# Performance work log

Measured on AMD Instinct MI355X. Metric: run time of the kernel, lower is better.

The kernel has to match this reference:

```python
import jax, jax.numpy as jnp
import numpy as np
import math

B, S, HID = 2, 2048, 2048
H, KVH, D = 16, 4, 128
EPS = 1e-6
THETA = 10000.0


def _rope_tables(key):
    inv_freq = 1.0 / (THETA ** (jnp.arange(0, D, 2, dtype=jnp.float32) / D))  # [D/2]
    pos = jnp.arange(S, dtype=jnp.float32)
    freqs = pos[:, None] * inv_freq[None, :]            # [S, D/2]
    emb = jnp.concatenate([freqs, freqs], axis=-1)      # [S, D]
    cos = jnp.broadcast_to(jnp.cos(emb)[None], (B, S, D))
    sin = jnp.broadcast_to(jnp.sin(emb)[None], (B, S, D))
    return cos, sin


def setup_inputs() -> dict:
    key = jax.random.key(0)
    ks = jax.random.split(key, 6)
    hidden_states = jax.random.normal(ks[0], (B, S, HID), dtype=jnp.float32)
    # causal additive mask, broadcastable to [B, H, S, S]
    causal = jnp.tril(jnp.ones((S, S), dtype=jnp.bool_))
    attention_mask = jnp.where(causal, 0.0, jnp.finfo(jnp.float32).min)[None, None]
    cos, sin = _rope_tables(key)
    sc = 0.02
    Wq = jax.random.normal(ks[1], (HID, H * D), dtype=jnp.float32) * sc
    Wk = jax.random.normal(ks[2], (HID, KVH * D), dtype=jnp.float32) * sc
    Wv = jax.random.normal(ks[3], (HID, KVH * D), dtype=jnp.float32) * sc
    Wo = jax.random.normal(ks[4], (H * D, HID), dtype=jnp.float32) * sc
    q_norm_w = jnp.ones((D,), dtype=jnp.float32)
    k_norm_w = jnp.ones((D,), dtype=jnp.float32)
    return dict(hidden_states=hidden_states, attention_mask=attention_mask,
                cos=cos, sin=sin, Wq=Wq, Wk=Wk, Wv=Wv, Wo=Wo,
                q_norm_w=q_norm_w, k_norm_w=k_norm_w)


def _rms_norm(x, w, eps=EPS):
    dt = x.dtype
    xf = x.astype(jnp.float32)
    var = jnp.mean(xf * xf, axis=-1, keepdims=True)
    return (w * (xf * jax.lax.rsqrt(var + eps)).astype(dt)).astype(dt)


def _rotate_half(x):
    x1, x2 = jnp.split(x, 2, axis=-1)
    return jnp.concatenate([-x2, x1], axis=-1)


def reference(hidden_states, attention_mask, cos, sin, Wq, Wk, Wv, Wo, q_norm_w, k_norm_w):
    b, s, _ = hidden_states.shape
    q = (hidden_states @ Wq).reshape(b, s, H, D)
    k = (hidden_states @ Wk).reshape(b, s, KVH, D)
    v = (hidden_states @ Wv).reshape(b, s, KVH, D)
    q = _rms_norm(q, q_norm_w).transpose(0, 2, 1, 3)   # [B,H,S,D]
    k = _rms_norm(k, k_norm_w).transpose(0, 2, 1, 3)   # [B,KVH,S,D]
    v = v.transpose(0, 2, 1, 3)
    # RoPE: cos/sin [B,S,D] -> unsqueeze head dim
    c = cos[:, None]
    sn = sin[:, None]
    q = q * c + _rotate_half(q) * sn
    k = k * c + _rotate_half(k) * sn
    # repeat_kv for GQA
    n_rep = H // KVH
    k = jnp.repeat(k, n_rep, axis=1)
    v = jnp.repeat(v, n_rep, axis=1)
    scores = jnp.einsum('bhqd,bhkd->bhqk', q, k) / math.sqrt(D)
    scores = scores + attention_mask
    attn = jax.nn.softmax(scores.astype(jnp.float32), axis=-1).astype(q.dtype)
    out = jnp.einsum('bhqk,bhkd->bhqd', attn, v)
    out = out.transpose(0, 2, 1, 3).reshape(b, s, H * D)
    return out @ Wo
```

## Files before the change

### kernel.cpp

```cpp
#include <hip/hip_runtime.h>
#include <math.h>

#define B_ 2
#define S_ 2048
#define HID_ 2048
#define H_ 16
#define KVH_ 4
#define D_ 128

typedef __bf16 bf16x8 __attribute__((ext_vector_type(8)));
typedef float f32x4 __attribute__((ext_vector_type(4)));

__device__ __forceinline__ unsigned short f2bf(float x) {
  union { float f; unsigned u; } cv;
  cv.f = x;
  unsigned u = cv.u;
  u += 0x7FFFu + ((u >> 16) & 1u);
  return (unsigned short)(u >> 16);
}

__global__ __launch_bounds__(256) void convert_bf16_kernel(
    const float* __restrict__ in, unsigned short* __restrict__ out) {
  const size_t i = ((size_t)blockIdx.x * 256 + threadIdx.x) * 8;
  const float4 v0 = *reinterpret_cast<const float4*>(&in[i]);
  const float4 v1 = *reinterpret_cast<const float4*>(&in[i + 4]);
  ushort4 o0, o1;
  o0.x = f2bf(v0.x); o0.y = f2bf(v0.y); o0.z = f2bf(v0.z); o0.w = f2bf(v0.w);
  o1.x = f2bf(v1.x); o1.y = f2bf(v1.y); o1.z = f2bf(v1.z); o1.w = f2bf(v1.w);
  *reinterpret_cast<ushort4*>(&out[i]) = o0;
  *reinterpret_cast<ushort4*>(&out[i + 4]) = o1;
}

__global__ __launch_bounds__(256) void transpose_w_kernel(
    const float* __restrict__ Wq, const float* __restrict__ Wk,
    const float* __restrict__ Wv, const float* __restrict__ Wo,
    unsigned short* __restrict__ WqT, unsigned short* __restrict__ WkT,
    unsigned short* __restrict__ WvT, unsigned short* __restrict__ WoT) {
  int blk = blockIdx.x;
  const float* src;
  unsigned short* dst;
  int N;
  if (blk < 4096)      { src = Wq; dst = WqT; N = 2048; }
  else if (blk < 5120) { src = Wk; dst = WkT; N = 512;  blk -= 4096; }
  else if (blk < 6144) { src = Wv; dst = WvT; N = 512;  blk -= 5120; }
  else                 { src = Wo; dst = WoT; N = 2048; blk -= 6144; }
  const int tiles_n = N >> 5;
  const int ti = blk / tiles_n;
  const int tj = blk % tiles_n;

  __shared__ unsigned short T[32][40];
  const int t = threadIdx.x;
  const int r = t >> 3;
  const int c4 = (t & 7) * 4;

  const float4 v = *reinterpret_cast<const float4*>(
      &src[(size_t)(ti * 32 + r) * N + tj * 32 + c4]);
  T[r][c4 + 0] = f2bf(v.x);
  T[r][c4 + 1] = f2bf(v.y);
  T[r][c4 + 2] = f2bf(v.z);
  T[r][c4 + 3] = f2bf(v.w);
  __syncthreads();

  ushort4 o;
  o.x = T[c4 + 0][r];
  o.y = T[c4 + 1][r];
  o.z = T[c4 + 2][r];
  o.w = T[c4 + 3][r];
  *reinterpret_cast<ushort4*>(&dst[(size_t)(tj * 32 + r) * 2048 + ti * 32 + c4]) = o;
}

template <int MODE>
__device__ __forceinline__ void mfma_gemm_body(
    const unsigned short* __restrict__ A, const unsigned short* __restrict__ BT,
    float* __restrict__ C, int M, int N, int K, int NH, int bx, int by) {
  __shared__ unsigned short As[128][72];
  __shared__ unsigned short Bs[128][72];

  const int tid = threadIdx.x;
  const int m0 = by * 128, n0 = bx * 128;
  const int lane = tid & 63;
  const int wave = tid >> 6;
  const int wm = (wave >> 1) * 64;
  const int wn = (wave & 1) * 64;
  const int lr = lane & 15;
  const int lg = lane >> 4;

  const int srow = tid >> 2;
  const int skq = (tid & 3) * 8;

  const unsigned short* aptr = A + (size_t)(m0 + srow) * K + skq;
  const unsigned short* bptr = BT + (size_t)(n0 + srow) * K + skq;
  const size_t rstep = (size_t)64 * K;

  f32x4 acc[4][4];
#pragma unroll
  for (int i = 0; i < 4; ++i)
#pragma unroll
    for (int j = 0; j < 4; ++j)
#pragma unroll
      for (int r = 0; r < 4; ++r) acc[i][j][r] = 0.0f;

  for (int k0 = 0; k0 < K; k0 += 32) {
    const uint4 ga0 = *reinterpret_cast<const uint4*>(aptr + k0);
    const uint4 ga1 = *reinterpret_cast<const uint4*>(aptr + rstep + k0);
    const uint4 gb0 = *reinterpret_cast<const uint4*>(bptr + k0);
    const uint4 gb1 = *reinterpret_cast<const uint4*>(bptr + rstep + k0);
    __syncthreads();
    *reinterpret_cast<uint4*>(&As[srow][skq]) = ga0;
    *reinterpret_cast<uint4*>(&As[srow + 64][skq]) = ga1;
    *reinterpret_cast<uint4*>(&Bs[srow][skq]) = gb0;
    *reinterpret_cast<uint4*>(&Bs[srow + 64][skq]) = gb1;
    __syncthreads();

    bf16x8 af[4], bfr[4];
#pragma unroll
    for (int i = 0; i < 4; ++i) {
      af[i] = *reinterpret_cast<const bf16x8*>(&As[wm + i * 16 + lr][lg * 8]);
      bfr[i] = *reinterpret_cast<const bf16x8*>(&Bs[wn + i * 16 + lr][lg * 8]);
    }
#pragma unroll
    for (int i = 0; i < 4; ++i)
#pragma unroll
      for (int j = 0; j < 4; ++j)
        acc[i][j] = __builtin_amdgcn_mfma_f32_16x16x32_bf16(
            af[i], bfr[j], acc[i][j], 0, 0, 0);
  }

#pragma unroll
  for (int i = 0; i < 4; ++i) {
#pragma unroll
    for (int j = 0; j < 4; ++j) {
#pragma unroll
      for (int r = 0; r < 4; ++r) {
        const int m = m0 + wm + i * 16 + lg * 4 + r;
        const int n = n0 + wn + j * 16 + lr;
        const float val = acc[i][j][r];
        if (MODE == 0) {
          C[(size_t)m * N + n] = val;
        } else {
          const int b = m >> 11, s = m & (S_ - 1);
          const int h = n >> 7, d = n & 127;
          const size_t idx = (((size_t)b * NH + h) * S_ + s) * D_ + d;
          if (MODE == 1) {
            C[idx] = val;
          } else {
            reinterpret_cast<unsigned short*>(C)[idx] = f2bf(val);
          }
        }
      }
    }
  }
}

__global__ __launch_bounds__(256) void qkv_gemm_kernel(
    const unsigned short* __restrict__ hsb, const unsigned short* __restrict__ WqT,
    const unsigned short* __restrict__ WkT, const unsigned short* __restrict__ WvT,
    float* __restrict__ q, float* __restrict__ k, unsigned short* __restrict__ vb) {
  const int blk = blockIdx.x;
  if (blk < 512) {
    mfma_gemm_body<1>(hsb, WqT, q, B_ * S_, H_ * D_, HID_, H_, blk & 15, blk >> 4);
  } else if (blk < 640) {
    const int t = blk - 512;
    mfma_gemm_body<1>(hsb, WkT, k, B_ * S_, KVH_ * D_, HID_, KVH_, t & 3, t >> 2);
  } else {
    const int t = blk - 640;
    mfma_gemm_body<2>(hsb, WvT, reinterpret_cast<float*>(vb),
                      B_ * S_, KVH_ * D_, HID_, KVH_, t & 3, t >> 2);
  }
}

__global__ __launch_bounds__(256) void out_gemm_kernel(
    const unsigned short* __restrict__ A, const unsigned short* __restrict__ BT,
    float* __restrict__ C) {
  mfma_gemm_body<0>(A, BT, C, B_ * S_, HID_, H_ * D_, 0, blockIdx.x, blockIdx.y);
}

__global__ __launch_bounds__(256) void norm_rope_kernel(
    const float* __restrict__ q, const float* __restrict__ k,
    unsigned short* __restrict__ qb, unsigned short* __restrict__ kb,
    const float* __restrict__ cosb, const float* __restrict__ sinb,
    const float* __restrict__ qw, const float* __restrict__ kw) {
  const int wave = threadIdx.x >> 6;
  const int lane = threadIdx.x & 63;
  const int row = blockIdx.x * 4 + wave;
  const int rows_q = B_ * S_ * H_;

  const float* p;
  unsigned short* po;
  const float* w;
  int b, s;
  if (row < rows_q) {
    p = q + (size_t)row * D_;
    po = qb + (size_t)row * D_;
    w = qw;
    b = row / (H_ * S_);
    s = row & (S_ - 1);
  } else {
    const int r = row - rows_q;
    p = k + (size_t)r * D_;
    po = kb + (size_t)r * D_;
    w = kw;
    b = r / (KVH_ * S_);
    s = r & (S_ - 1);
  }

  const float x1 = p[lane];
  const float x2 = p[lane + 64];
  float ss = x1 * x1 + x2 * x2;
#pragma unroll
  for (int off = 32; off; off >>= 1) ss += __shfl_xor(ss, off, 64);
  const float inv = rsqrtf(ss * (1.0f / D_) + 1e-6f);
  const float xn1 = x1 * inv * w[lane];
  const float xn2 = x2 * inv * w[lane + 64];

  const size_t cb = ((size_t)b * S_ + s) * D_;
  const float c1 = cosb[cb + lane], c2 = cosb[cb + lane + 64];
  const float s1 = sinb[cb + lane], s2 = sinb[cb + lane + 64];
  po[lane]      = f2bf(xn1 * c1 - xn2 * s1);
  po[lane + 64] = f2bf(xn2 * c2 + xn1 * s2);
}

__global__ __launch_bounds__(256, 2) void attn_mfma_kernel(
    const unsigned short* __restrict__ qb, const unsigned short* __restrict__ kb,
    const unsigned short* __restrict__ vb, unsigned short* __restrict__ aob) {
  const int p = blockIdx.x;
  int u, bh;
  if (p < 256) { u = p & 15; bh = p >> 4; }
  else { const int pq = p - 256; u = 15 - (pq & 15); bh = 16 + (pq >> 4); }
  const int qta = u;
  const int qtb = 31 - u;
  const int b = bh >> 4;
  const int h = bh & 15;
  const int kvh = h >> 2;

  const int tid = threadIdx.x;
  const int wv = tid >> 6;
  const int lane = tid & 63;
  const int lr = lane & 15;
  const int kg = lane >> 4;

  __shared__ unsigned short Ks[64 * 128];
  __shared__ unsigned short VT[128 * 64];
  __shared__ unsigned short Ps[64 * 64];

  const unsigned short* qbaseA =
      qb + (((size_t)b * H_ + h) * S_ + (size_t)qta * 64) * D_;
  const unsigned short* qbaseB =
      qb + (((size_t)b * H_ + h) * S_ + (size_t)qtb * 64) * D_;
  const unsigned short* kbase = kb + (((size_t)b * KVH_ + kvh) * S_) * D_;
  const unsigned short* vbase = vb + (((size_t)b * KVH_ + kvh) * S_) * D_;

  bf16x8 qfa[4], qfb[4];
#pragma unroll
  for (int ks = 0; ks < 4; ++ks) {
    qfa[ks] = *reinterpret_cast<const bf16x8*>(
        qbaseA + (size_t)(wv * 16 + lr) * D_ + ks * 32 + kg * 8);
    qfb[ks] = *reinterpret_cast<const bf16x8*>(
        qbaseB + (size_t)(wv * 16 + lr) * D_ + ks * 32 + kg * 8);
  }

  f32x4 oa[8], ob[8];
#pragma unroll
  for (int d0 = 0; d0 < 8; ++d0)
#pragma unroll
    for (int r = 0; r < 4; ++r) { oa[d0][r] = 0.0f; ob[d0][r] = 0.0f; }
  float ma[4] = {-1e30f, -1e30f, -1e30f, -1e30f};
  float la[4] = {0.0f, 0.0f, 0.0f, 0.0f};
  float mb[4] = {-1e30f, -1e30f, -1e30f, -1e30f};
  float lb[4] = {0.0f, 0.0f, 0.0f, 0.0f};
  const float scale = 0.08838834764831845f;

  const int krow = tid >> 4;
  const int kc8 = (tid & 15) * 8;
  const int vjp = tid & 31;
  const int vd4b = tid >> 5;

  uint4 kr[4];
  ushort4 vr0[4], vr1[4];

#pragma unroll
  for (int it = 0; it < 4; ++it) {
    kr[it] = *reinterpret_cast<const uint4*>(
        kbase + (size_t)(it * 16 + krow) * D_ + kc8);
    const int d4 = (it * 8 + vd4b) * 4;
    vr0[it] = *reinterpret_cast<const ushort4*>(
        vbase + (size_t)(2 * vjp) * D_ + d4);
    vr1[it] = *reinterpret_cast<const ushort4*>(
        vbase + (size_t)(2 * vjp + 1) * D_ + d4);
  }

  const int last = qtb;

  auto compute_tile = [&](const bf16x8* qf, f32x4* o, float* m_run,
                          float* l_run, int qtile, int kt) {
    f32x4 s[4];
#pragma unroll
    for (int j = 0; j < 4; ++j)
#pragma unroll
      for (int r = 0; r < 4; ++r) s[j][r] = 0.0f;
    __builtin_amdgcn_s_setprio(1);
#pragma unroll
    for (int ks = 0; ks < 4; ++ks) {
#pragma unroll
      for (int j = 0; j < 4; ++j) {
        const int krw = j * 16 + lr;
        const bf16x8 kf = *reinterpret_cast<const bf16x8*>(
            &Ks[krw * 128 + ((ks * 32 + kg * 8) ^ ((krw & 7) * 8))]);
        s[j] = __builtin_amdgcn_mfma_f32_16x16x32_bf16(qf[ks], kf, s[j], 0, 0, 0);
      }
    }
    __builtin_amdgcn_s_setprio(0);

    if (kt == qtile) {
      const int qrow0 = wv * 16 + kg * 4;
#pragma unroll
      for (int j = 0; j < 4; ++j) {
        const int kcol = j * 16 + lr;
#pragma unroll
        for (int r = 0; r < 4; ++r)
          s[j][r] = (kcol <= qrow0 + r) ? s[j][r] * scale : -1e30f;
      }
    } else {
#pragma unroll
      for (int j = 0; j < 4; ++j)
#pragma unroll
        for (int r = 0; r < 4; ++r) s[j][r] *= scale;
    }

#pragma unroll
    for (int r = 0; r < 4; ++r) {
      float mx = fmaxf(fmaxf(s[0][r], s[1][r]), fmaxf(s[2][r], s[3][r]));
      mx = fmaxf(mx, __shfl_xor(mx, 1));
      mx = fmaxf(mx, __shfl_xor(mx, 2));
      mx = fmaxf(mx, __shfl_xor(mx, 4));
      mx = fmaxf(mx, __shfl_xor(mx, 8));
      const float mn = fmaxf(m_run[r], mx);
      const float al = __expf(m_run[r] - mn);
      float sum = 0.0f;
#pragma unroll
      for (int j = 0; j < 4; ++j) {
        s[j][r] = __expf(s[j][r] - mn);
        sum += s[j][r];
      }
      sum += __shfl_xor(sum, 1);
      sum += __shfl_xor(sum, 2);
      sum += __shfl_xor(sum, 4);
      sum += __shfl_xor(sum, 8);
      l_run[r] = l_run[r] * al + sum;
      m_run[r] = mn;
#pragma unroll
      for (int d0 = 0; d0 < 8; ++d0) o[d0][r] *= al;
    }

#pragma unroll
    for (int r = 0; r < 4; ++r) {
      const int prow = wv * 16 + kg * 4 + r;
      const int swz = (prow & 7) * 8;
#pragma unroll
      for (int j = 0; j < 4; ++j)
        Ps[prow * 64 + ((j * 16 + lr) ^ swz)] = f2bf(s[j][r]);
    }

    __builtin_amdgcn_s_setprio(1);
#pragma unroll
    for (int ks = 0; ks < 2; ++ks) {
      const int arow = wv * 16 + lr;
      const bf16x8 pf = *reinterpret_cast<const bf16x8*>(
          &Ps[arow * 64 + ((ks * 32 + kg * 8) ^ ((arow & 7) * 8))]);
#pragma unroll
      for (int d0 = 0; d0 < 8; ++d0) {
        const int vrow = d0 * 16 + lr;
        const bf16x8 vf = *reinterpret_cast<const bf16x8*>(
            &VT[vrow * 64 + ((ks * 32 + kg * 8) ^ ((vrow & 7) * 8))]);
        o[d0] = __builtin_amdgcn_mfma_f32_16x16x32_bf16(pf, vf, o[d0], 0, 0, 0);
      }
    }
    __builtin_amdgcn_s_setprio(0);
  };

  for (int kt = 0; kt <= last; ++kt) {
#pragma unroll
    for (int it = 0; it < 4; ++it) {
      const int r = it * 16 + krow;
      *reinterpret_cast<uint4*>(&Ks[r * 128 + (kc8 ^ ((r & 7) * 8))]) = kr[it];
      const int d4 = (it * 8 + vd4b) * 4;
      const int rsw = 2 * vjp;
      ushort2 w0, w1, w2, w3;
      w0.x = vr0[it].x; w0.y = vr1[it].x;
      w1.x = vr0[it].y; w1.y = vr1[it].y;
      w2.x = vr0[it].z; w2.y = vr1[it].z;
      w3.x = vr0[it].w; w3.y = vr1[it].w;
      *reinterpret_cast<ushort2*>(&VT[(d4 + 0) * 64 + (rsw ^ (((d4 + 0) & 7) * 8))]) = w0;
      *reinterpret_cast<ushort2*>(&VT[(d4 + 1) * 64 + (rsw ^ (((d4 + 1) & 7) * 8))]) = w1;
      *reinterpret_cast<ushort2*>(&VT[(d4 + 2) * 64 + (rsw ^ (((d4 + 2) & 7) * 8))]) = w2;
      *reinterpret_cast<ushort2*>(&VT[(d4 + 3) * 64 + (rsw ^ (((d4 + 3) & 7) * 8))]) = w3;
    }
    __syncthreads();

    if (kt < last) {
      const size_t koff = (size_t)(kt + 1) * 64;
#pragma unroll
      for (int it = 0; it < 4; ++it) {
        kr[it] = *reinterpret_cast<const uint4*>(
            kbase + (koff + it * 16 + krow) * D_ + kc8);
        const int d4 = (it * 8 + vd4b) * 4;
        vr0[it] = *reinterpret_cast<const ushort4*>(
            vbase + (koff + 2 * vjp) * D_ + d4);
        vr1[it] = *reinterpret_cast<const ushort4*>(
            vbase + (koff + 2 * vjp + 1) * D_ + d4);
      }
    }

    if (kt <= qta) compute_tile(qfa, oa, ma, la, qta, kt);
    compute_tile(qfb, ob, mb, lb, qtb, kt);
    __syncthreads();
  }

#pragma unroll
  for (int r = 0; r < 4; ++r) {
    const float inva = 1.0f / la[r];
    const float invb = 1.0f / lb[r];
    const size_t rowa = (size_t)b * S_ + (size_t)qta * 64 + wv * 16 + kg * 4 + r;
    const size_t rowb = (size_t)b * S_ + (size_t)qtb * 64 + wv * 16 + kg * 4 + r;
    unsigned short* opa = aob + rowa * (H_ * D_) + h * D_;
    unsigned short* opb = aob + rowb * (H_ * D_) + h * D_;
#pragma unroll
    for (int d0 = 0; d0 < 8; ++d0) {
      opa[d0 * 16 + lr] = f2bf(oa[d0][r] * inva);
      opb[d0 * 16 + lr] = f2bf(ob[d0][r] * invb);
    }
  }
}

extern "C" void kernel_launch(void* const* d_in, const int* in_sizes, int n_in,
                              void* d_out, int out_size, void* d_ws, size_t ws_size,
                              hipStream_t stream) {
  const float* hs   = (const float*)d_in[0];
  const float* cosb = (const float*)d_in[2];
  const float* sinb = (const float*)d_in[3];
  const float* Wq   = (const float*)d_in[4];
  const float* Wk   = (const float*)d_in[5];
  const float* Wv   = (const float*)d_in[6];
  const float* Wo   = (const float*)d_in[7];
  const float* qw   = (const float*)d_in[8];
  const float* kw   = (const float*)d_in[9];

  char* ws = (char*)d_ws;
  float* q  = (float*)ws;                     ws += (size_t)8388608 * 4;
  float* k  = (float*)ws;                     ws += (size_t)2097152 * 4;
  unsigned short* qbb = (unsigned short*)ws;  ws += (size_t)8388608 * 2;
  unsigned short* kbb = (unsigned short*)ws;  ws += (size_t)2097152 * 2;
  unsigned short* vbb = (unsigned short*)ws;  ws += (size_t)2097152 * 2;
  unsigned short* hsb = (unsigned short*)ws;  ws += (size_t)8388608 * 2;
  unsigned short* WqT = (unsigned short*)ws;  ws += (size_t)4194304 * 2;
  unsigned short* WkT = (unsigned short*)ws;  ws += (size_t)1048576 * 2;
  unsigned short* WvT = (unsigned short*)ws;  ws += (size_t)1048576 * 2;
  unsigned short* WoT = (unsigned short*)ws;  ws += (size_t)4194304 * 2;
  unsigned short* aob = (unsigned short*)ws;  ws += (size_t)8388608 * 2;
  float* out = (float*)d_out;

  const dim3 blk(256);

  convert_bf16_kernel<<<dim3(4096), blk, 0, stream>>>(hs, hsb);
  transpose_w_kernel<<<dim3(10240), blk, 0, stream>>>(
      Wq, Wk, Wv, Wo, WqT, WkT, WvT, WoT);

  qkv_gemm_kernel<<<dim3(768), blk, 0, stream>>>(hsb, WqT, WkT, WvT, q, k, vbb);

  norm_rope_kernel<<<dim3((B_ * S_ * (H_ + KVH_)) / 4), blk, 0, stream>>>(
      q, k, qbb, kbb, cosb, sinb, qw, kw);

  attn_mfma_kernel<<<dim3(512), blk, 0, stream>>>(qbb, kbb, vbb, aob);

  out_gemm_kernel<<<dim3(HID_ / 128, (B_ * S_) / 128), blk, 0, stream>>>(
      aob, WoT, out);
}
```

Before: 430.5 us.

## Use direct global-to-LDS loads in GEMM and split P buffers in attention

The projection GEMM now stages its A and B tiles through global_load_lds builtins that write straight into shared memory, with an unpadded 32-wide layout, instead of loading into registers and storing to LDS. This removes the register round trip and the VGPR pressure it causes. The unpadded layout may bring LDS bank conflicts on the fragment reads. The attention kernel also gives each of its two query tiles its own P scratch buffer, which removes a hidden write-after-read hazard between the two compute_tile calls and costs 8KB more LDS.

```diff
diff --git a/kernel.cpp b/kernel.cpp
--- a/kernel.cpp
+++ b/kernel.cpp
@@ -17,6 +17,13 @@
   unsigned u = cv.u;
   u += 0x7FFFu + ((u >> 16) & 1u);
   return (unsigned short)(u >> 16);
+}
+
+__device__ __forceinline__ void gload_lds16(const unsigned short* g,
+                                            unsigned short* l) {
+  __builtin_amdgcn_global_load_lds(
+      (const __attribute__((address_space(1))) unsigned int*)g,
+      (__attribute__((address_space(3))) unsigned int*)l, 16, 0, 0);
 }
 
 __global__ __launch_bounds__(256) void convert_bf16_kernel(
@@ -73,8 +80,8 @@
 __device__ __forceinline__ void mfma_gemm_body(
     const unsigned short* __restrict__ A, const unsigned short* __restrict__ BT,
     float* __restrict__ C, int M, int N, int K, int NH, int bx, int by) {
-  __shared__ unsigned short As[128][72];
-  __shared__ unsigned short Bs[128][72];
+  __shared__ unsigned short As[128 * 32];
+  __shared__ unsigned short Bs[128 * 32];
 
   const int tid = threadIdx.x;
   const int m0 = by * 128, n0 = bx * 128;
@@ -85,12 +92,16 @@
   const int lr = lane & 15;
   const int lg = lane >> 4;
 
-  const int srow = tid >> 2;
-  const int skq = (tid & 3) * 8;
-
-  const unsigned short* aptr = A + (size_t)(m0 + srow) * K + skq;
-  const unsigned short* bptr = BT + (size_t)(n0 + srow) * K + skq;
-  const size_t rstep = (size_t)64 * K;
+  const int sgrow = wave * 32 + (lane >> 2);
+  const int sgcol = (lane & 3) * 8;
+  const unsigned short* gA0 = A + (size_t)(m0 + sgrow) * K + sgcol;
+  const unsigned short* gA1 = A + (size_t)(m0 + sgrow + 16) * K + sgcol;
+  const unsigned short* gB0 = BT + (size_t)(n0 + sgrow) * K + sgcol;
+  const unsigned short* gB1 = BT + (size_t)(n0 + sgrow + 16) * K + sgcol;
+  unsigned short* lA0 = As + (size_t)(wave * 32) * 32;
+  unsigned short* lA1 = As + (size_t)(wave * 32 + 16) * 32;
+  unsigned short* lB0 = Bs + (size_t)(wave * 32) * 32;
+  unsigned short* lB1 = Bs + (size_t)(wave * 32 + 16) * 32;
 
   f32x4 acc[4][4];
 #pragma unroll
@@ -101,22 +112,18 @@
       for (int r = 0; r < 4; ++r) acc[i][j][r] = 0.0f;
 
   for (int k0 = 0; k0 < K; k0 += 32) {
-    const uint4 ga0 = *reinterpret_cast<const uint4*>(aptr + k0);
-    const uint4 ga1 = *reinterpret_cast<const uint4*>(aptr + rstep + k0);
-    const uint4 gb0 = *reinterpret_cast<const uint4*>(bptr + k0);
-    const uint4 gb1 = *reinterpret_cast<const uint4*>(bptr + rstep + k0);
     __syncthreads();
-    *reinterpret_cast<uint4*>(&As[srow][skq]) = ga0;
-    *reinterpret_cast<uint4*>(&As[srow + 64][skq]) = ga1;
-    *reinterpret_cast<uint4*>(&Bs[srow][skq]) = gb0;
-    *reinterpret_cast<uint4*>(&Bs[srow + 64][skq]) = gb1;
+    gload_lds16(gA0 + k0, lA0);
+    gload_lds16(gA1 + k0, lA1);
+    gload_lds16(gB0 + k0, lB0);
+    gload_lds16(gB1 + k0, lB1);
     __syncthreads();
 
     bf16x8 af[4], bfr[4];
 #pragma unroll
     for (int i = 0; i < 4; ++i) {
-      af[i] = *reinterpret_cast<const bf16x8*>(&As[wm + i * 16 + lr][lg * 8]);
-      bfr[i] = *reinterpret_cast<const bf16x8*>(&Bs[wn + i * 16 + lr][lg * 8]);
+      af[i] = *reinterpret_cast<const bf16x8*>(&As[(wm + i * 16 + lr) * 32 + lg * 8]);
+      bfr[i] = *reinterpret_cast<const bf16x8*>(&Bs[(wn + i * 16 + lr) * 32 + lg * 8]);
     }
 #pragma unroll
     for (int i = 0; i < 4; ++i)
@@ -241,7 +248,8 @@
 
   __shared__ unsigned short Ks[64 * 128];
   __shared__ unsigned short VT[128 * 64];
-  __shared__ unsigned short Ps[64 * 64];
+  __shared__ unsigned short PsA[64 * 64];
+  __shared__ unsigned short PsB[64 * 64];
 
   const unsigned short* qbaseA =
       qb + (((size_t)b * H_ + h) * S_ + (size_t)qta * 64) * D_;
@@ -292,7 +300,8 @@
   const int last = qtb;
 
   auto compute_tile = [&](const bf16x8* qf, f32x4* o, float* m_run,
-                          float* l_run, int qtile, int kt) {
+                          float* l_run, int qtile, int kt,
+                          unsigned short* Ps) {
     f32x4 s[4];
 #pragma unroll
     for (int j = 0; j < 4; ++j)
@@ -411,8 +420,8 @@
       }
     }
 
-    if (kt <= qta) compute_tile(qfa, oa, ma, la, qta, kt);
-    compute_tile(qfb, ob, mb, lb, qtb, kt);
+    if (kt <= qta) compute_tile(qfa, oa, ma, la, qta, kt, PsA);
+    compute_tile(qfb, ob, mb, lb, qtb, kt, PsB);
     __syncthreads();
   }
 
```

Result: no change. 424.7 us (-1.3%).
